# Performance work log

Measured on AMD Instinct MI355X. Metric: run time of the kernel, lower is better.

## Reference

```python
import jax, jax.numpy as jnp
import numpy as np

K = (0.3, 0.3, 0.4)   # args.args_k_0..2
EPS = 1e-8


def squash(v, axis=-1):
    norm = jnp.linalg.norm(v, axis=axis, keepdims=True)
    scale = norm ** 2 / (1.0 + norm ** 2) / (norm + EPS)
    return scale * v


def setup_inputs() -> dict:
    key = jax.random.key(0)
    kx, kw = jax.random.split(key)
    B, IN, DIN, OUT, DOUT = 128, 4608, 8, 10, 16
    x = jax.random.normal(kx, (B, IN, DIN), dtype=jnp.float32)
    weight = 0.1 * jax.random.normal(kw, (OUT, IN, DOUT, DIN), dtype=jnp.float32)
    return {"x": x, "weight": weight}


def reference(x, weight):
    # x: [B, I, Din], weight: [O, I, Dout, Din]
    # x_hat[b,o,i,d] = sum_k weight[o,i,d,k] * x[b,i,k]
    x_hat = jnp.einsum('oidk,bik->boid', weight, x)  # [B, O, I, Dout]
    x_hat_d = jax.lax.stop_gradient(x_hat)
    B, O, I, D = x_hat.shape
    b = jnp.zeros((B, O, I), dtype=x.dtype)
    feats = []
    for it in range(3):
        c = jax.nn.softmax(b, axis=1)[..., None]          # [B, O, I, 1], softmax over out caps
        if it == 2:
            out = squash(jnp.sum(c * x_hat, axis=-2, keepdims=True))      # [B, O, 1, D]
        else:
            out = squash(jnp.sum(c * x_hat_d, axis=-2, keepdims=True))    # [B, O, 1, D]
            b = b + jnp.sum(out * x_hat_d, axis=-1)                       # agreement update
        feats.append(out * K[it])
    # stack -> [3, B, O, 1, D]; squeeze caps-sum axis; sum over iterations
    outputs = jnp.sum(jnp.squeeze(jnp.stack(feats), axis=-2), axis=0)     # [B, O, D]
    return outputs.reshape(B, O, 4, 4)
```

## Files before the change

kernel.cpp:

```cpp
#include <hip/hip_runtime.h>

#define B_    128
#define I_    4608
#define O_    10
#define D_    16
#define NCHUNKS 2304
#define NIB   32
#define CPB   72
#define CHH   2560
#define PSET  20480

typedef _Float16 f16x2 __attribute__((ext_vector_type(2)));
typedef _Float16 f16x4 __attribute__((ext_vector_type(4)));
typedef _Float16 f16x8 __attribute__((ext_vector_type(8)));
typedef float    f32x4 __attribute__((ext_vector_type(4)));
typedef __fp16   pk16x2 __attribute__((ext_vector_type(2)));
typedef unsigned int uint2v __attribute__((ext_vector_type(2)));

__device__ __forceinline__ f16x4 pack4(float a, float b, float c, float d) {
    union { f16x4 v; pk16x2 p[2]; } u;
    u.p[0] = __builtin_amdgcn_cvt_pkrtz(a, b);
    u.p[1] = __builtin_amdgcn_cvt_pkrtz(c, d);
    return u.v;
}
__device__ __forceinline__ f16x2 splat_h2(float a) {
    union { f16x2 v; pk16x2 p; } u;
    u.p = __builtin_amdgcn_cvt_pkrtz(a, a);
    return u.v;
}

template<int MODE>
__global__ __launch_bounds__(512, 2)
void pass_kernel(const float* __restrict__ x,
                 const float* __restrict__ w,
                 _Float16* __restrict__ pwW,
                 const _Float16* __restrict__ pw,
                 const float* __restrict__ v,
                 float* __restrict__ parts)
{
    __shared__ float red[4 * 2560];

    const int tid  = threadIdx.x;
    const int lane = tid & 63;
    const int wv   = tid >> 6;
    const int bl   = lane & 15;
    const int g    = lane >> 4;
    const int u    = blockIdx.x;
    const int xcd  = u & 7, s = u >> 3;
    const int ib   = xcd * 4 + (s & 3);
    const int bg   = s >> 2;
    const int c0   = ib * CPB;
    const int iloc = g & 1, kq = g >> 1;
    const int b0   = bg * 16 + bl;
    const bool wrt = (MODE == 0) && (bg == 0);

    f16x4 idf;
#pragma unroll
    for (int j = 0; j < 4; ++j) idf[j] = (_Float16)((bl == 4 * g + j) ? 1.f : 0.f);

    f16x4 vf[O_];
    if (MODE == 1) {
#pragma unroll
        for (int o = 0; o < O_; ++o) {
            const float4 vv = *(const float4*)(v + ((long)b0 * O_ + o) * D_ + g * 4);
            vf[o] = pack4(vv.x, vv.y, vv.z, vv.w);
        }
    }

    f32x4 S[O_];
#pragma unroll
    for (int o = 0; o < O_; ++o) S[o] = (f32x4)(0.f);

    const long lofs = (long)lane * 8;
    const int  wofs = bl * 8 + kq * 4;
    auto fragp = [&](int c, int p) {
        return (const f16x8*)(pw + (long)c * CHH + p * 512 + lofs);
    };
    auto xp = [&](int c) {
        return (const float4*)(x + ((long)b0 * I_ + 2 * c + iloc) * 8 + kq * 4);
    };
    auto wload = [&](int c, f16x8 (&f)[5]) {
        const long iofs = (long)(2 * c + iloc) * 128 + wofs;
#pragma unroll
        for (int p = 0; p < 5; ++p) {
            const float4 w0 = *(const float4*)(w + (long)(2 * p)     * (I_ * 128) + iofs);
            const float4 w1 = *(const float4*)(w + (long)(2 * p + 1) * (I_ * 128) + iofs);
            union { f16x8 v8; f16x4 h[2]; } u2;
            u2.h[0] = pack4(w0.x, w0.y, w0.z, w0.w);
            u2.h[1] = pack4(w1.x, w1.y, w1.z, w1.w);
            f[p] = u2.v8;
        }
    };

    int c = c0 + wv;
    f16x8 f1[5];
    float4 xqC, xqN;
    if (MODE == 0) wload(c, f1);
    else {
#pragma unroll
        for (int p = 0; p < 5; ++p) f1[p] = *fragp(c, p);
    }
    xqC = *xp(c);

    for (int t5 = 0; t5 < 9; ++t5) {
        int cn = c + 8; if (cn > NCHUNKS - 1) cn = NCHUNKS - 1;
        xqN = *xp(cn);

        float cs[O_];
        if (MODE == 1) {
#pragma unroll
            for (int p = 0; p < 5; ++p) {
                f16x4 pe, po;
                pe[0]=f1[p][0]; pe[1]=f1[p][1]; pe[2]=f1[p][2]; pe[3]=f1[p][3];
                po[0]=f1[p][4]; po[1]=f1[p][5]; po[2]=f1[p][6]; po[3]=f1[p][7];
                const f32x4 te = __builtin_amdgcn_mfma_f32_16x16x16f16(pe, idf, (f32x4)(0.f), 0, 0, 0);
                const f32x4 to = __builtin_amdgcn_mfma_f32_16x16x16f16(po, idf, (f32x4)(0.f), 0, 0, 0);
                const f16x4 ae = pack4(te[0], te[1], te[2], te[3]);
                const f16x4 ao = pack4(to[0], to[1], to[2], to[3]);
                const f32x4 ua = __builtin_amdgcn_mfma_f32_16x16x16f16(ae, vf[2*p],   (f32x4)(0.f), 0, 0, 0);
                const f32x4 ub = __builtin_amdgcn_mfma_f32_16x16x16f16(ao, vf[2*p+1], (f32x4)(0.f), 0, 0, 0);
                float d0 = ua[0] * xqC.x; d0 = fmaf(ua[1], xqC.y, d0);
                d0 = fmaf(ua[2], xqC.z, d0); d0 = fmaf(ua[3], xqC.w, d0);
                float d1 = ub[0] * xqC.x; d1 = fmaf(ub[1], xqC.y, d1);
                d1 = fmaf(ub[2], xqC.z, d1); d1 = fmaf(ub[3], xqC.w, d1);
                cs[2*p] = d0; cs[2*p+1] = d1;
            }
            float ssum = 0.f;
#pragma unroll
            for (int o = 0; o < O_; ++o) {
                const unsigned int tt = __float_as_uint(cs[o]);
                const uint2v sw = __builtin_amdgcn_permlane32_swap(tt, tt, false, false);
                const float e = __expf(__uint_as_float(sw[0]) + __uint_as_float(sw[1]));
                cs[o] = e; ssum += e;
            }
            const float inv = 1.f / ssum;
#pragma unroll
            for (int o = 0; o < O_; ++o) cs[o] *= inv;
        }

        union F4 { f16x4 v; f16x2 h[2]; };
        F4 xh;
        xh.v = pack4(xqC.x, xqC.y, xqC.z, xqC.w);
#pragma unroll
        for (int p = 0; p < 5; ++p) {
            f16x4 pe, po;
            pe[0]=f1[p][0]; pe[1]=f1[p][1]; pe[2]=f1[p][2]; pe[3]=f1[p][3];
            po[0]=f1[p][4]; po[1]=f1[p][5]; po[2]=f1[p][6]; po[3]=f1[p][7];
            F4 ye, yo;
            if (MODE == 0) { ye = xh; yo = xh; }
            else {
                const f16x2 ce = splat_h2(cs[2*p]);
                const f16x2 co = splat_h2(cs[2*p+1]);
                ye.h[0] = xh.h[0] * ce; ye.h[1] = xh.h[1] * ce;
                yo.h[0] = xh.h[0] * co; yo.h[1] = xh.h[1] * co;
            }
            S[2*p]   = __builtin_amdgcn_mfma_f32_16x16x16f16(pe, ye.v, S[2*p],   0, 0, 0);
            S[2*p+1] = __builtin_amdgcn_mfma_f32_16x16x16f16(po, yo.v, S[2*p+1], 0, 0, 0);
        }

        if (MODE == 0) {
            if (wrt) {
#pragma unroll
                for (int p = 0; p < 5; ++p)
                    *(f16x8*)(pwW + (long)c * CHH + p * 512 + lofs) = f1[p];
            }
            wload(cn, f1);
        } else {
#pragma unroll
            for (int p = 0; p < 5; ++p) f1[p] = *fragp(cn, p);
        }
        xqC = xqN;
        c += 8;
    }

    auto slot = [&](int ww, int o) {
        return &red[ww * 2560 + o * 256 + lane * 4];
    };
#define TREE_WR(WSRC)                                                       \
    if (wv >= WSRC && wv < 2 * WSRC) {                                      \
        _Pragma("unroll") for (int o = 0; o < O_; ++o)                      \
            *(f32x4*)slot(wv - WSRC, o) = S[o];                             \
    }                                                                       \
    __syncthreads();                                                        \
    if (wv < WSRC) {                                                        \
        _Pragma("unroll") for (int o = 0; o < O_; ++o)                      \
            S[o] += *(f32x4*)slot(wv, o);                                   \
    }                                                                       \
    __syncthreads();

    TREE_WR(4)
    TREE_WR(2)
    TREE_WR(1)
#undef TREE_WR

    if (wv == 0) {
#pragma unroll
        for (int o = 0; o < O_; ++o) {
            float* pp = parts + (long)ib * PSET + ((long)b0 * O_ + o) * D_ + g * 4;
            *(f32x4*)pp = S[o];
        }
    }
}

__global__ __launch_bounds__(256)
void reduce_squash(const float* __restrict__ parts, float* __restrict__ v_buf,
                   float* __restrict__ out, float kscale, float pre, int mode)
{
    __shared__ float red2[4][16];
    const int tid  = threadIdx.x;
    const int lane = tid & 63;
    const int wv   = tid >> 6;
    const int g2   = blockIdx.x;
    const int pg   = tid >> 4;
    const int d    = tid & 15;

    float s = 0.f;
#pragma unroll
    for (int k = 0; k < 2; ++k)
        s += parts[(long)(pg * 2 + k) * PSET + g2 * D_ + d];

    s += __shfl_xor(s, 16);
    s += __shfl_xor(s, 32);
    if (lane < 16) red2[wv][lane] = s;
    __syncthreads();

    if (tid < 16) {
        float tot = (red2[0][tid] + red2[1][tid]) + (red2[2][tid] + red2[3][tid]);
        tot *= pre;
        float n2 = tot * tot;
        n2 += __shfl_xor(n2, 1);
        n2 += __shfl_xor(n2, 2);
        n2 += __shfl_xor(n2, 4);
        n2 += __shfl_xor(n2, 8);
        const float n     = sqrtf(n2);
        const float scale = n2 / ((1.f + n2) * (n + 1e-8f));
        const float o_    = scale * tot;
        const int idx = g2 * D_ + tid;
        if (mode == 0)      { v_buf[idx] = o_;  out[idx]  = kscale * o_; }
        else if (mode == 1) { v_buf[idx] += o_; out[idx] += kscale * o_; }
        else                {                   out[idx] += kscale * o_; }
    }
}

extern "C" void kernel_launch(void* const* d_in, const int* in_sizes, int n_in,
                              void* d_out, int out_size, void* d_ws, size_t ws_size,
                              hipStream_t stream)
{
    const float* x = (const float*)d_in[0];
    const float* w = (const float*)d_in[1];
    float* out   = (float*)d_out;
    float* parts = (float*)d_ws;
    float* v_buf = parts + (long)NIB * PSET;
    _Float16* pw = (_Float16*)(v_buf + B_ * O_ * D_);

    pass_kernel<0><<<256, 512, 0, stream>>>(x, w, pw, pw, v_buf, parts);
    reduce_squash<<<1280, 256, 0, stream>>>(parts, v_buf, out, 0.3f, 0.1f, 0);

    pass_kernel<1><<<256, 512, 0, stream>>>(x, w, pw, pw, v_buf, parts);
    reduce_squash<<<1280, 256, 0, stream>>>(parts, v_buf, out, 0.3f, 1.0f, 1);

    pass_kernel<1><<<256, 512, 0, stream>>>(x, w, pw, pw, v_buf, parts);
    reduce_squash<<<1280, 256, 0, stream>>>(parts, v_buf, out, 0.4f, 1.0f, 2);
}
```

Measured before the change: 61.51 us.

## Fuse per-iteration reduce+squash into next pass prologue, single final squash

Removes the two intermediate reduce_squash launches. Each routing pass now reduces the 32 per-block partials for its 16-row batch group, squashes them and rebuilds v in LDS at kernel start. Partials are stored transposed (ib innermost) so each prologue reads contiguous 32-float runs. One final kernel squashes all three iterations and writes the output. The cost is redundant reduction work, since every block re-reduces its group's partials, plus extra barriers and strided scalar stores of the partials.

```diff
diff --git a/kernel.cpp b/kernel.cpp
--- a/kernel.cpp
+++ b/kernel.cpp
@@ -8,7 +8,8 @@
 #define NIB   32
 #define CPB   72
 #define CHH   2560
-#define PSET  20480
+#define UPS   20480
+#define PSTRIDE ((long)UPS * NIB)
 
 typedef _Float16 f16x2 __attribute__((ext_vector_type(2)));
 typedef _Float16 f16x4 __attribute__((ext_vector_type(4)));
@@ -28,15 +29,26 @@
     u.p = __builtin_amdgcn_cvt_pkrtz(a, a);
     return u.v;
 }
-
-template<int MODE>
+__device__ __forceinline__ float sum32(const float* p) {
+    const float4* p4 = (const float4*)p;
+    float4 a = p4[0], b = p4[1], c = p4[2], d = p4[3];
+    float4 e = p4[4], f = p4[5], g = p4[6], h = p4[7];
+    float s0 = (a.x+a.y)+(a.z+a.w), s1 = (b.x+b.y)+(b.z+b.w);
+    float s2 = (c.x+c.y)+(c.z+c.w), s3 = (d.x+d.y)+(d.z+d.w);
+    float s4 = (e.x+e.y)+(e.z+e.w), s5 = (f.x+f.y)+(f.z+f.w);
+    float s6 = (g.x+g.y)+(g.z+g.w), s7 = (h.x+h.y)+(h.z+h.w);
+    return ((s0+s1)+(s2+s3))+((s4+s5)+(s6+s7));
+}
+
+template<int ITER>
 __global__ __launch_bounds__(512, 2)
 void pass_kernel(const float* __restrict__ x,
                  const float* __restrict__ w,
                  _Float16* __restrict__ pwW,
                  const _Float16* __restrict__ pw,
-                 const float* __restrict__ v,
-                 float* __restrict__ parts)
+                 const float* __restrict__ parts0,
+                 const float* __restrict__ parts1,
+                 float* __restrict__ partsOut)
 {
     __shared__ float red[4 * 2560];
 
@@ -52,19 +64,56 @@
     const int c0   = ib * CPB;
     const int iloc = g & 1, kq = g >> 1;
     const int b0   = bg * 16 + bl;
-    const bool wrt = (MODE == 0) && (bg == 0);
+    const int bb   = bg * 16;
+    const bool wrt = (ITER == 0) && (bg == 0);
 
     f16x4 idf;
 #pragma unroll
     for (int j = 0; j < 4; ++j) idf[j] = (_Float16)((bl == 4 * g + j) ? 1.f : 0.f);
 
+    float* a0  = red;
+    float* sc0 = red + 2576;
+    float* a1  = red + 2736;
+    float* sc1 = red + 5312;
     f16x4 vf[O_];
-    if (MODE == 1) {
+    if (ITER >= 1) {
+#pragma unroll
+        for (int q = 0; q < 5; ++q) {
+            const int uq   = tid + q * 512;
+            const int bloc = uq / 160, rem = uq - bloc * 160;
+            const long gofs = ((long)bb * 160 + uq) * NIB;
+            a0[bloc * 161 + rem] = 0.1f * sum32(parts0 + gofs);
+            if (ITER == 2) a1[bloc * 161 + rem] = sum32(parts1 + gofs);
+        }
+        __syncthreads();
+        if (tid < 160) {
+            const int base = (tid / 10) * 161 + (tid % 10) * 16;
+            float n2 = 0.f;
+#pragma unroll
+            for (int d = 0; d < 16; ++d) { const float t = a0[base + d]; n2 = fmaf(t, t, n2); }
+            sc0[tid] = n2 / ((1.f + n2) * (sqrtf(n2) + 1e-8f));
+            if (ITER == 2) {
+                float m2 = 0.f;
+#pragma unroll
+                for (int d = 0; d < 16; ++d) { const float t = a1[base + d]; m2 = fmaf(t, t, m2); }
+                sc1[tid] = m2 / ((1.f + m2) * (sqrtf(m2) + 1e-8f));
+            }
+        }
+        __syncthreads();
 #pragma unroll
         for (int o = 0; o < O_; ++o) {
-            const float4 vv = *(const float4*)(v + ((long)b0 * O_ + o) * D_ + g * 4);
-            vf[o] = pack4(vv.x, vv.y, vv.z, vv.w);
-        }
+            const int base = bl * 161 + o * 16 + 4 * g;
+            const float s0v = sc0[bl * 10 + o];
+            float v0 = a0[base] * s0v, v1 = a0[base + 1] * s0v;
+            float v2 = a0[base + 2] * s0v, v3 = a0[base + 3] * s0v;
+            if (ITER == 2) {
+                const float s1v = sc1[bl * 10 + o];
+                v0 = fmaf(a1[base], s1v, v0);     v1 = fmaf(a1[base + 1], s1v, v1);
+                v2 = fmaf(a1[base + 2], s1v, v2); v3 = fmaf(a1[base + 3], s1v, v3);
+            }
+            vf[o] = pack4(v0, v1, v2, v3);
+        }
+        __syncthreads();
     }
 
     f32x4 S[O_];
@@ -95,7 +144,7 @@
     int c = c0 + wv;
     f16x8 f1[5];
     float4 xqC, xqN;
-    if (MODE == 0) wload(c, f1);
+    if (ITER == 0) wload(c, f1);
     else {
 #pragma unroll
         for (int p = 0; p < 5; ++p) f1[p] = *fragp(c, p);
@@ -107,7 +156,7 @@
         xqN = *xp(cn);
 
         float cs[O_];
-        if (MODE == 1) {
+        if (ITER >= 1) {
 #pragma unroll
             for (int p = 0; p < 5; ++p) {
                 f16x4 pe, po;
@@ -147,7 +196,7 @@
             pe[0]=f1[p][0]; pe[1]=f1[p][1]; pe[2]=f1[p][2]; pe[3]=f1[p][3];
             po[0]=f1[p][4]; po[1]=f1[p][5]; po[2]=f1[p][6]; po[3]=f1[p][7];
             F4 ye, yo;
-            if (MODE == 0) { ye = xh; yo = xh; }
+            if (ITER == 0) { ye = xh; yo = xh; }
             else {
                 const f16x2 ce = splat_h2(cs[2*p]);
                 const f16x2 co = splat_h2(cs[2*p+1]);
@@ -158,7 +207,7 @@
             S[2*p+1] = __builtin_amdgcn_mfma_f32_16x16x16f16(po, yo.v, S[2*p+1], 0, 0, 0);
         }
 
-        if (MODE == 0) {
+        if (ITER == 0) {
             if (wrt) {
 #pragma unroll
                 for (int p = 0; p < 5; ++p)
@@ -173,6 +222,7 @@
         c += 8;
     }
 
+    __syncthreads();
     auto slot = [&](int ww, int o) {
         return &red[ww * 2560 + o * 256 + lane * 4];
     };
@@ -196,50 +246,54 @@
     if (wv == 0) {
 #pragma unroll
         for (int o = 0; o < O_; ++o) {
-            float* pp = parts + (long)ib * PSET + ((long)b0 * O_ + o) * D_ + g * 4;
-            *(f32x4*)pp = S[o];
+            const long base = ((long)(b0 * 10 + o) * 16 + 4 * g) * NIB + ib;
+            partsOut[base]           = S[o][0];
+            partsOut[base + NIB]     = S[o][1];
+            partsOut[base + 2 * NIB] = S[o][2];
+            partsOut[base + 3 * NIB] = S[o][3];
         }
     }
 }
 
 __global__ __launch_bounds__(256)
-void reduce_squash(const float* __restrict__ parts, float* __restrict__ v_buf,
-                   float* __restrict__ out, float kscale, float pre, int mode)
+void final_squash(const float* __restrict__ p0, const float* __restrict__ p1,
+                  const float* __restrict__ p2, float* __restrict__ out)
 {
     __shared__ float red2[4][16];
     const int tid  = threadIdx.x;
     const int lane = tid & 63;
     const int wv   = tid >> 6;
-    const int g2   = blockIdx.x;
+    const int unit = blockIdx.x;
+    const int d    = tid & 15;
     const int pg   = tid >> 4;
-    const int d    = tid & 15;
-
-    float s = 0.f;
-#pragma unroll
-    for (int k = 0; k < 2; ++k)
-        s += parts[(long)(pg * 2 + k) * PSET + g2 * D_ + d];
-
-    s += __shfl_xor(s, 16);
-    s += __shfl_xor(s, 32);
-    if (lane < 16) red2[wv][lane] = s;
-    __syncthreads();
-
-    if (tid < 16) {
-        float tot = (red2[0][tid] + red2[1][tid]) + (red2[2][tid] + red2[3][tid]);
-        tot *= pre;
-        float n2 = tot * tot;
-        n2 += __shfl_xor(n2, 1);
-        n2 += __shfl_xor(n2, 2);
-        n2 += __shfl_xor(n2, 4);
-        n2 += __shfl_xor(n2, 8);
-        const float n     = sqrtf(n2);
-        const float scale = n2 / ((1.f + n2) * (n + 1e-8f));
-        const float o_    = scale * tot;
-        const int idx = g2 * D_ + tid;
-        if (mode == 0)      { v_buf[idx] = o_;  out[idx]  = kscale * o_; }
-        else if (mode == 1) { v_buf[idx] += o_; out[idx] += kscale * o_; }
-        else                {                   out[idx] += kscale * o_; }
-    }
+
+    const float pres[3] = {0.1f, 1.f, 1.f};
+    const float ks[3]   = {0.3f, 0.3f, 0.4f};
+    const float* ps[3]  = {p0, p1, p2};
+
+    float acc = 0.f;
+#pragma unroll
+    for (int setk = 0; setk < 3; ++setk) {
+        const float* pp = ps[setk] + ((long)unit * 16 + d) * NIB + pg * 2;
+        float sv = pp[0] + pp[1];
+        sv += __shfl_xor(sv, 16);
+        sv += __shfl_xor(sv, 32);
+        if (lane < 16) red2[wv][lane] = sv;
+        __syncthreads();
+        if (tid < 16) {
+            float tot = (red2[0][tid] + red2[1][tid]) + (red2[2][tid] + red2[3][tid]);
+            tot *= pres[setk];
+            float n2 = tot * tot;
+            n2 += __shfl_xor(n2, 1);
+            n2 += __shfl_xor(n2, 2);
+            n2 += __shfl_xor(n2, 4);
+            n2 += __shfl_xor(n2, 8);
+            const float n = sqrtf(n2);
+            acc = fmaf(ks[setk] * (n2 / ((1.f + n2) * (n + 1e-8f))), tot, acc);
+        }
+        __syncthreads();
+    }
+    if (tid < 16) out[unit * D_ + tid] = acc;
 }
 
 extern "C" void kernel_launch(void* const* d_in, const int* in_sizes, int n_in,
@@ -248,17 +302,14 @@
 {
     const float* x = (const float*)d_in[0];
     const float* w = (const float*)d_in[1];
-    float* out   = (float*)d_out;
-    float* parts = (float*)d_ws;
-    float* v_buf = parts + (long)NIB * PSET;
-    _Float16* pw = (_Float16*)(v_buf + B_ * O_ * D_);
-
-    pass_kernel<0><<<256, 512, 0, stream>>>(x, w, pw, pw, v_buf, parts);
-    reduce_squash<<<1280, 256, 0, stream>>>(parts, v_buf, out, 0.3f, 0.1f, 0);
-
-    pass_kernel<1><<<256, 512, 0, stream>>>(x, w, pw, pw, v_buf, parts);
-    reduce_squash<<<1280, 256, 0, stream>>>(parts, v_buf, out, 0.3f, 1.0f, 1);
-
-    pass_kernel<1><<<256, 512, 0, stream>>>(x, w, pw, pw, v_buf, parts);
-    reduce_squash<<<1280, 256, 0, stream>>>(parts, v_buf, out, 0.4f, 1.0f, 2);
-}
+    float* out    = (float*)d_out;
+    float* parts0 = (float*)d_ws;
+    float* parts1 = parts0 + PSTRIDE;
+    float* parts2 = parts1 + PSTRIDE;
+    _Float16* pw  = (_Float16*)(parts2 + PSTRIDE);
+
+    pass_kernel<0><<<256, 512, 0, stream>>>(x, w, pw, pw, parts0, parts1, parts0);
+    pass_kernel<1><<<256, 512, 0, stream>>>(x, w, pw, pw, parts0, parts1, parts1);
+    pass_kernel<2><<<256, 512, 0, stream>>>(x, w, pw, pw, parts0, parts1, parts2);
+    final_squash<<<1280, 256, 0, stream>>>(parts0, parts1, parts2, out);
+}
```

Measured after the change: 94.29 us. 1.53x slower.
